# Kernel optimization log

Hardware: AMD Instinct MI355X
Metric: run time of the kernel (lower is better)

Reference implementation:

```python
import jax, jax.numpy as jnp
import numpy as np

M, N, NUM_ITER, BATCH = 512, 2048, 16, 4096


def setup_inputs() -> dict:
    key = jax.random.key(0)
    k_y, k_D, k_thr = jax.random.split(key, 3)
    # Dictionary D (== A in the module), column-scaled like a sensing matrix
    D = np.asarray(jax.random.normal(k_D, (M, N), dtype=jnp.float32)) / np.sqrt(M)
    # W = inv(D D^T) D, then normalize columns so w_i . d_i == 1 (ALISTA analytic weight)
    W = np.linalg.inv(D @ D.T) @ D
    W = W / np.sum(W * D, axis=0, keepdims=True)
    y = jax.random.normal(k_y, (BATCH, M), dtype=jnp.float32)
    thr = jax.random.uniform(k_thr, (NUM_ITER,), dtype=jnp.float32) * 0.1  # positive thresholds
    step = jnp.ones((NUM_ITER,), dtype=jnp.float32)
    return {"y": y, "A": jnp.asarray(D), "W": jnp.asarray(W), "thr": thr, "step": step}


def reference(y, A, W, thr, step):
    # y: [B, m]; A, W: [m, n]; thr, step: [numIter]
    B = y.shape[0]
    n = A.shape[1]

    def body(d, ts):
        t, s = ts
        r = d @ A.T - y                      # [B, m]  == (A @ d.T - y.T).T
        z = d - s * (r @ W)                  # [B, n]  == (W.T @ r.T).T
        d_new = jnp.sign(z) * jnp.maximum(jnp.abs(z) - t, 0.0)  # soft threshold
        return d_new, d_new

    d0 = jnp.zeros((B, n), dtype=y.dtype)
    _, xs = jax.lax.scan(body, d0, (thr, step))
    return xs  # [numIter, B, n]: all intermediate iterates, like the returned list x
```

## Files before the change

### kernel.cpp

```cpp
#include <hip/hip_runtime.h>


#define NDIM 2048
#define MDIM 512
#define BATCHN 4096
#define NITER 16

#define BM2 256
#define BN2 128
#define BK3 64

typedef _Float16 f16;
typedef f16 f16x8 __attribute__((ext_vector_type(8)));
typedef float f32x4 __attribute__((ext_vector_type(4)));

__device__ __forceinline__ void gload_lds16(const void* g, void* lds) {
  __builtin_amdgcn_global_load_lds(
      (const __attribute__((address_space(1))) unsigned int*)g,
      (__attribute__((address_space(3))) unsigned int*)lds, 16, 0, 0);
}

template <int EPI, int NK>
__global__ __launch_bounds__(512, 2) void gemm_phased(
    const f16* __restrict__ Aop, const f16* __restrict__ Bop,
    const f16* __restrict__ Ds, const f16* __restrict__ Ch,
    const float* __restrict__ thr, const float* __restrict__ step, int it,
    float sigma, float inv_sigma, float inv_sigma_next,
    float* __restrict__ outIter, f16* __restrict__ DsNext,
    f16* __restrict__ outH)
{
  constexpr int K = NK * BK3;
  __shared__ __align__(16) f16 ldsAll[3 * BM2 * BK3 + 3 * BN2 * BK3];
  f16* ldsA = ldsAll;
  f16* ldsB = ldsAll + 3 * BM2 * BK3;

  const int tid = threadIdx.x;
  const int w = tid >> 6, l = tid & 63;
  const int ks = w & 1;
  const int wn = (w >> 1) & 1;
  const int wm = w >> 2;
  const int h = l >> 4;

  const int bid = blockIdx.x;
  const int cpx = (int)(gridDim.x >> 3);
  const int wgid = (bid & 7) * cpx + (bid >> 3);
  const int rowTile = (wgid >> 4) * BM2;
  const int colTile = (wgid & 15) * BN2;

  const f16* Abase = Aop + (size_t)rowTile * K;
  const f16* Bbase = Bop + (size_t)colTile * K;

  auto stageA = [&](int buf, int t, int r) {
    int row = r * 64 + (tid >> 3);
    int gsw = ((tid & 7) ^ (row & 7)) << 4;
    gload_lds16((const char*)(Abase + (size_t)row * K + t * BK3) + gsw,
                (char*)ldsA + buf * 32768 + r * 8192 + w * 1024);
  };
  auto stageB = [&](int buf, int t, int r) {
    int row = r * 64 + (tid >> 3);
    int gsw = ((tid & 7) ^ (row & 7)) << 4;
    gload_lds16((const char*)(Bbase + (size_t)row * K + t * BK3) + gsw,
                (char*)ldsB + buf * 16384 + r * 8192 + w * 1024);
  };

#define READ_A4(bR, mOfs, af)                                                   \
  {                                                                             \
    const f16* bA_ = ldsA + (bR) * 16384;                                       \
    const int c_ = ks * 4 + h;                                                  \
    _Pragma("unroll")                                                           \
    for (int m = 0; m < 4; ++m) {                                               \
      int row = wm * 128 + ((mOfs) + m) * 16 + (l & 15);                        \
      af[m] = *(const f16x8*)(bA_ + row * 64 + ((c_ ^ (row & 7)) << 3));        \
    }                                                                           \
  }
#define READ_B4(bR, bf)                                                         \
  {                                                                             \
    const f16* bB_ = ldsB + (bR) * 8192;                                        \
    const int c_ = ks * 4 + h;                                                  \
    _Pragma("unroll")                                                           \
    for (int n = 0; n < 4; ++n) {                                               \
      int row = wn * 64 + n * 16 + (l & 15);                                    \
      bf[n] = *(const f16x8*)(bB_ + row * 64 + ((c_ ^ (row & 7)) << 3));        \
    }                                                                           \
  }

#define MFMA16(accOfs, af, bf)                                                  \
  __builtin_amdgcn_s_setprio(1);                                                \
  _Pragma("unroll")                                                             \
  for (int m = 0; m < 4; ++m)                                                   \
    _Pragma("unroll")                                                           \
    for (int n = 0; n < 4; ++n)                                                 \
      acc[(accOfs) + m][n] = __builtin_amdgcn_mfma_f32_16x16x32_f16(            \
          af[m], bf[n], acc[(accOfs) + m][n], 0, 0, 0);                         \
  __builtin_amdgcn_s_setprio(0);

  f32x4 acc[8][4] = {};
  f16x8 af[4], bf[4];

#pragma unroll
  for (int r = 0; r < 4; ++r) stageA(0, 0, r);
#pragma unroll
  for (int r = 0; r < 2; ++r) stageB(0, 0, r);
#pragma unroll
  for (int r = 0; r < 4; ++r) stageA(1, 1, r);
#pragma unroll
  for (int r = 0; r < 2; ++r) stageB(1, 1, r);
  asm volatile("s_waitcnt vmcnt(6)" ::: "memory");
  __builtin_amdgcn_s_barrier();
  __builtin_amdgcn_sched_barrier(0);

  int bR = 0;
  int bS = 2;

  for (int t = 0; t < NK; ++t) {
    const bool pf = (t + 2 < NK);

    READ_A4(bR, 0, af);
    READ_B4(bR, bf);
    if (pf) { stageA(bS, t + 2, 0); stageA(bS, t + 2, 1); stageB(bS, t + 2, 0); }
    __builtin_amdgcn_s_barrier();
    asm volatile("s_waitcnt lgkmcnt(0)" ::: "memory");
    __builtin_amdgcn_sched_barrier(0);
    MFMA16(0, af, bf);
    __builtin_amdgcn_s_barrier();

    READ_A4(bR, 4, af);
    if (pf) { stageA(bS, t + 2, 2); stageA(bS, t + 2, 3); stageB(bS, t + 2, 1); }
    __builtin_amdgcn_s_barrier();
    asm volatile("s_waitcnt lgkmcnt(0)" ::: "memory");
    __builtin_amdgcn_sched_barrier(0);
    MFMA16(4, af, bf);
    if (pf) asm volatile("s_waitcnt vmcnt(6)" ::: "memory");
    else    asm volatile("s_waitcnt vmcnt(0)" ::: "memory");
    __builtin_amdgcn_s_barrier();
    __builtin_amdgcn_sched_barrier(0);

    bR = (bR == 2) ? 0 : bR + 1;
    bS = (bS == 2) ? 0 : bS + 1;
  }

  float* xb = (float*)ldsAll;
  const int p = w >> 1;
  const size_t sbase = (size_t)p * 8192 + (size_t)ks * 4096;
  const size_t rbase = (size_t)p * 8192 + (size_t)(ks ^ 1) * 4096;
  if (ks == 0) {
#pragma unroll
    for (int m4 = 0; m4 < 4; ++m4)
#pragma unroll
      for (int n = 0; n < 4; ++n)
        *(f32x4*)(xb + sbase + l * 64 + (((m4 * 4 + n) ^ (l & 15)) << 2)) = acc[4 + m4][n];
  } else {
#pragma unroll
    for (int m4 = 0; m4 < 4; ++m4)
#pragma unroll
      for (int n = 0; n < 4; ++n)
        *(f32x4*)(xb + sbase + l * 64 + (((m4 * 4 + n) ^ (l & 15)) << 2)) = acc[m4][n];
  }
  __syncthreads();
  if (ks == 0) {
#pragma unroll
    for (int m4 = 0; m4 < 4; ++m4)
#pragma unroll
      for (int n = 0; n < 4; ++n)
        acc[m4][n] += *(const f32x4*)(xb + rbase + l * 64 + (((m4 * 4 + n) ^ (l & 15)) << 2));
  } else {
#pragma unroll
    for (int m4 = 0; m4 < 4; ++m4)
#pragma unroll
      for (int n = 0; n < 4; ++n)
        acc[4 + m4][n] += *(const f32x4*)(xb + rbase + l * 64 + (((m4 * 4 + n) ^ (l & 15)) << 2));
  }

  const int baseRow = rowTile + wm * 128 + ks * 64 + (h << 2);
  const int baseCol = colTile + wn * 64 + (l & 15);
  float s = 0.f, tt = 0.f;
  size_t itOff = 0;
  if (EPI >= 1) {
    s = step[it];
    tt = thr[it];
    itOff = (size_t)it * (size_t)BATCHN * NDIM;
  }
#define EPILOG(ACCOFS)                                                          \
  _Pragma("unroll")                                                             \
  for (int m4 = 0; m4 < 4; ++m4)                                                \
    _Pragma("unroll")                                                           \
    for (int n = 0; n < 4; ++n)                                                 \
      _Pragma("unroll")                                                         \
      for (int r = 0; r < 4; ++r) {                                             \
        int row = baseRow + m4 * 16 + r;                                        \
        int col = baseCol + n * 16;                                             \
        size_t g = (size_t)row * NDIM + col;                                    \
        float v = acc[(ACCOFS) + m4][n][r];                                     \
        if (EPI == 0) {                                                         \
          outH[g] = (f16)v;                                                     \
        } else if (EPI == 1) {                                                  \
          outH[g] = (f16)v;                                                     \
          float z = s * v;                                                      \
          float az = __builtin_fabsf(z) - tt;                                   \
          float dn = az > 0.f ? (z > 0.f ? az : -az) : 0.f;                     \
          outIter[g] = dn;                                                      \
          DsNext[g] = (f16)dn;                                                  \
        } else {                                                                \
          float ds = (float)Ds[g];                                              \
          float cv = (float)Ch[g];                                              \
          float z = sigma * (ds - s * (v - cv * inv_sigma));                    \
          float az = __builtin_fabsf(z) - tt;                                   \
          float dn = az > 0.f ? (z > 0.f ? az : -az) : 0.f;                     \
          outIter[itOff + g] = dn;                                              \
          DsNext[g] = (f16)(dn * inv_sigma_next);                               \
        }                                                                       \
      }
  if (ks == 0) { EPILOG(0) } else { EPILOG(4) }
#undef EPILOG
#undef READ_A4
#undef READ_B4
#undef MFMA16
}

__global__ __launch_bounds__(256) void trans_h(
    const float* __restrict__ in, f16* __restrict__ oh)
{
  __shared__ float tile[64][65];
  int t = threadIdx.x;
  int tr = t >> 6;
  int tc = t & 63;
  int r0 = blockIdx.y * 64;
  int c0 = blockIdx.x * 64;
#pragma unroll
  for (int i = 0; i < 16; ++i) {
    int r = i * 4 + tr;
    tile[r][tc] = in[(size_t)(r0 + r) * NDIM + c0 + tc];
  }
  __syncthreads();
#pragma unroll
  for (int i = 0; i < 16; ++i) {
    int r = i * 4 + tr;
    oh[(size_t)(c0 + r) * MDIM + r0 + tc] = (f16)tile[tc][r];
  }
}

__global__ __launch_bounds__(256) void tofp16(
    const float* __restrict__ in, f16* __restrict__ oh)
{
  size_t i = (size_t)blockIdx.x * 256 + threadIdx.x;
  oh[i] = (f16)in[i];
}

extern "C" void kernel_launch(void* const* d_in, const int* in_sizes, int n_in,
                              void* d_out, int out_size, void* d_ws, size_t ws_size,
                              hipStream_t stream)
{
  const float* y    = (const float*)d_in[0];
  const float* A    = (const float*)d_in[1];
  const float* W    = (const float*)d_in[2];
  const float* thr  = (const float*)d_in[3];
  const float* step = (const float*)d_in[4];
  float* out = (float*)d_out;
  char* ws = (char*)d_ws;

  f16* Pht = (f16*)(ws + 0);
  f16* Ch  = (f16*)(ws + (8ull  << 20));
  f16* DsA = (f16*)(ws + (24ull << 20));
  f16* DsB = (f16*)(ws + (40ull << 20));
  f16* Wth = (f16*)(ws + (40ull << 20));
  f16* Ath = (f16*)(ws + (42ull << 20));
  f16* yh  = (f16*)(ws + (44ull << 20));

  trans_h<<<dim3(32, 8), 256, 0, stream>>>(A, Ath);
  trans_h<<<dim3(32, 8), 256, 0, stream>>>(W, Wth);
  tofp16<<<(BATCHN * MDIM) / 256, 256, 0, stream>>>(y, yh);

  gemm_phased<0, MDIM / BK3><<<dim3(128), 512, 0, stream>>>(
      Wth, Ath, nullptr, nullptr, thr, step, 0,
      0.f, 0.f, 0.f, nullptr, nullptr, Pht);

  gemm_phased<1, MDIM / BK3><<<dim3(256), 512, 0, stream>>>(
      yh, Wth, nullptr, nullptr, thr, step, 0,
      0.f, 0.f, 1.0f, out, DsA, Ch);

  f16* cur = DsA;
  f16* nxt = DsB;
  float sigma = 1.0f;
  for (int it = 1; it < NITER; ++it) {
    gemm_phased<2, NDIM / BK3><<<dim3(256), 512, 0, stream>>>(
        cur, Pht, cur, Ch, thr, step, it,
        sigma, 1.0f / sigma, 0.25f / sigma, out, nxt, nullptr);
    sigma *= 4.0f;
    f16* tmp = cur; cur = nxt; nxt = tmp;
  }
}
```

Baseline: 733.9 us.

## Merge GEMM K-step into single phase and fuse preprocessing kernels

The GEMM main loop now reads both A halves into separate register sets and issues all prefetch stages up front, removing one barrier pair per K-step and using a partial lgkmcnt wait so the first MFMA group can start while the second A-half loads. The three preprocessing kernels (two transposes and the fp16 cast of y) are merged into one launch that splits work by block index, saving two launch overheads. The trade is extra register pressure from the second A fragment set, and prefetch issue that is now bunched rather than spread across the step.

```diff
diff --git a/kernel.cpp b/kernel.cpp
--- a/kernel.cpp
+++ b/kernel.cpp
@@ -95,7 +95,7 @@
   __builtin_amdgcn_s_setprio(0);
 
   f32x4 acc[8][4] = {};
-  f16x8 af[4], bf[4];
+  f16x8 afE[4], afO[4], bf[4];
 
 #pragma unroll
   for (int r = 0; r < 4; ++r) stageA(0, 0, r);
@@ -115,21 +115,22 @@
   for (int t = 0; t < NK; ++t) {
     const bool pf = (t + 2 < NK);
 
-    READ_A4(bR, 0, af);
+    READ_A4(bR, 0, afE);
     READ_B4(bR, bf);
-    if (pf) { stageA(bS, t + 2, 0); stageA(bS, t + 2, 1); stageB(bS, t + 2, 0); }
+    READ_A4(bR, 4, afO);
+    if (pf) {
+      stageA(bS, t + 2, 0); stageA(bS, t + 2, 1);
+      stageA(bS, t + 2, 2); stageA(bS, t + 2, 3);
+      stageB(bS, t + 2, 0); stageB(bS, t + 2, 1);
+    }
+    __builtin_amdgcn_sched_barrier(0);
     __builtin_amdgcn_s_barrier();
+    asm volatile("s_waitcnt lgkmcnt(4)" ::: "memory");
+    __builtin_amdgcn_sched_barrier(0);
+    MFMA16(0, afE, bf);
     asm volatile("s_waitcnt lgkmcnt(0)" ::: "memory");
     __builtin_amdgcn_sched_barrier(0);
-    MFMA16(0, af, bf);
-    __builtin_amdgcn_s_barrier();
-
-    READ_A4(bR, 4, af);
-    if (pf) { stageA(bS, t + 2, 2); stageA(bS, t + 2, 3); stageB(bS, t + 2, 1); }
-    __builtin_amdgcn_s_barrier();
-    asm volatile("s_waitcnt lgkmcnt(0)" ::: "memory");
-    __builtin_amdgcn_sched_barrier(0);
-    MFMA16(4, af, bf);
+    MFMA16(4, afO, bf);
     if (pf) asm volatile("s_waitcnt vmcnt(6)" ::: "memory");
     else    asm volatile("s_waitcnt vmcnt(0)" ::: "memory");
     __builtin_amdgcn_s_barrier();
@@ -217,33 +218,39 @@
 #undef MFMA16
 }
 
-__global__ __launch_bounds__(256) void trans_h(
-    const float* __restrict__ in, f16* __restrict__ oh)
+__global__ __launch_bounds__(256) void preprep(
+    const float* __restrict__ A, const float* __restrict__ W,
+    const float* __restrict__ y,
+    f16* __restrict__ Ath, f16* __restrict__ Wth, f16* __restrict__ yh)
 {
-  __shared__ float tile[64][65];
+  int b = blockIdx.x;
   int t = threadIdx.x;
-  int tr = t >> 6;
-  int tc = t & 63;
-  int r0 = blockIdx.y * 64;
-  int c0 = blockIdx.x * 64;
-#pragma unroll
-  for (int i = 0; i < 16; ++i) {
-    int r = i * 4 + tr;
-    tile[r][tc] = in[(size_t)(r0 + r) * NDIM + c0 + tc];
-  }
-  __syncthreads();
-#pragma unroll
-  for (int i = 0; i < 16; ++i) {
-    int r = i * 4 + tr;
-    oh[(size_t)(c0 + r) * MDIM + r0 + tc] = (f16)tile[tc][r];
-  }
-}
-
-__global__ __launch_bounds__(256) void tofp16(
-    const float* __restrict__ in, f16* __restrict__ oh)
-{
-  size_t i = (size_t)blockIdx.x * 256 + threadIdx.x;
-  oh[i] = (f16)in[i];
+  if (b < 512) {
+    const float* in = (b < 256) ? A : W;
+    f16* oh = (b < 256) ? Ath : Wth;
+    int bb = b & 255;
+    __shared__ float tile[64][65];
+    int tr = t >> 6;
+    int tc = t & 63;
+    int r0 = (bb >> 5) * 64;
+    int c0 = (bb & 31) * 64;
+#pragma unroll
+    for (int i = 0; i < 16; ++i) {
+      int r = i * 4 + tr;
+      tile[r][tc] = in[(size_t)(r0 + r) * NDIM + c0 + tc];
+    }
+    __syncthreads();
+#pragma unroll
+    for (int i = 0; i < 16; ++i) {
+      int r = i * 4 + tr;
+      oh[(size_t)(c0 + r) * MDIM + r0 + tc] = (f16)tile[tc][r];
+    }
+  } else {
+    size_t base = (size_t)(b - 512) * 256 * 32 + t;
+#pragma unroll
+    for (int i = 0; i < 32; ++i)
+      yh[base + i * 256] = (f16)y[base + i * 256];
+  }
 }
 
 extern "C" void kernel_launch(void* const* d_in, const int* in_sizes, int n_in,
@@ -266,9 +273,7 @@
   f16* Ath = (f16*)(ws + (42ull << 20));
   f16* yh  = (f16*)(ws + (44ull << 20));
 
-  trans_h<<<dim3(32, 8), 256, 0, stream>>>(A, Ath);
-  trans_h<<<dim3(32, 8), 256, 0, stream>>>(W, Wth);
-  tofp16<<<(BATCHN * MDIM) / 256, 256, 0, stream>>>(y, yh);
+  preprep<<<dim3(768), 256, 0, stream>>>(A, W, y, Ath, Wth, yh);
 
   gemm_phased<0, MDIM / BK3><<<dim3(128), 512, 0, stream>>>(
       Wth, Ath, nullptr, nullptr, thr, step, 0,
```

Measured after the change: 745.0 us. About the same (+1.5%).
